# Optimization experiments

Measured on AMD Instinct MI355X. Metric: run time of the kernel, lower is better.

Reference implementation:

```python
import jax, jax.numpy as jnp
import numpy as np

N_NODES = 50_000
EMB = 128
N_GROUPS = 100_000
PER_GROUP = 8
E = N_GROUPS * PER_GROUP  # 800_000


def setup_inputs() -> dict:
    key = jax.random.key(0)
    ks = jax.random.split(key, 12)
    h = 2 * EMB
    inp = {
        "repr": jax.random.normal(ks[0], (N_NODES, EMB), jnp.float32),
        "gd": jax.random.randint(ks[1], (E,), 0, N_NODES, jnp.int32),
        "gd_len": jnp.full((N_GROUPS,), PER_GROUP, jnp.int32),
        "gd_deg": jax.random.uniform(ks[2], (E,), jnp.float32) * 8.0,
        # mlp_combine_gd_deg: Linear(emb+1 -> 2emb), ReLU, Linear(2emb -> emb)
        "W1c": jax.random.normal(ks[3], (EMB + 1, h), jnp.float32) / np.sqrt(EMB + 1),
        "b1c": jnp.zeros((h,), jnp.float32),
        "W2c": jax.random.normal(ks[4], (h, EMB), jnp.float32) / np.sqrt(h),
        "b2c": jnp.zeros((EMB,), jnp.float32),
        # mlp_gd_process: Linear(emb -> 2emb), ReLU, Linear(2emb -> emb)
        "W1p": jax.random.normal(ks[5], (EMB, h), jnp.float32) / np.sqrt(EMB),
        "b1p": jnp.zeros((h,), jnp.float32),
        "W2p": jax.random.normal(ks[6], (h, EMB), jnp.float32) / np.sqrt(h),
        "b2p": jnp.zeros((EMB,), jnp.float32),
    }
    return inp


def reference(repr, gd, gd_len, gd_deg, W1c, b1c, W2c, b2c, W1p, b1p, W2p, b2p):
    n_groups = gd_len.shape[0]
    total = gd.shape[0]
    # gather node reprs along the geodesic index list: [E, emb]
    gd_repr = repr[gd]
    # mlp_combine_gd_deg on [gd_repr ; deg]: [E, emb+1] -> [E, 2emb] -> [E, emb]
    x = jnp.concatenate([gd_repr, gd_deg[:, None]], axis=-1)
    hidden = jax.nn.relu(x @ W1c + b1c)
    gd_repr = hidden @ W2c + b2c
    # count_to_group_index(gd_len): repeat group id i gd_len[i] times, then scatter-add
    group_idx = jnp.repeat(jnp.arange(n_groups, dtype=jnp.int32), gd_len,
                           total_repeat_length=total)
    seg = jax.ops.segment_sum(gd_repr, group_idx, num_segments=n_groups)  # [G, emb]
    # mlp_gd_process
    out = jax.nn.relu(seg @ W1p + b1p) @ W2p + b2p
    return out
```

## Files before the change

kernel.cpp:

```cpp
#include <hip/hip_runtime.h>

typedef _Float16 f16;
typedef _Float16 f16x4 __attribute__((ext_vector_type(4)));
typedef _Float16 f16x8 __attribute__((ext_vector_type(8)));
typedef float f32x4 __attribute__((ext_vector_type(4)));

#define GRID 512

static __device__ __forceinline__ f32x4 mfma16(f16x8 a, f16x8 b, f32x4 c) {
  return __builtin_amdgcn_mfma_f32_16x16x32_f16(a, b, c, 0, 0, 0);
}

__global__ void prep_kernel(const float* __restrict__ W1c, const float* __restrict__ W2c,
                            const float* __restrict__ W1p, const float* __restrict__ W2p,
                            f16* __restrict__ wt) {
  int h = blockIdx.x * 256 + threadIdx.x;
  int local = h & 32767;
  float v;
  if (h < 32768)      { int n = local >> 7, k = local & 127; v = W1c[k * 256 + n]; }
  else if (h < 65536) { int n = local >> 8, k = local & 255; v = W2c[k * 128 + n]; }
  else if (h < 98304) { int n = local >> 7, k = local & 127; v = W1p[k * 256 + n]; }
  else                { int n = local >> 8, k = local & 255; v = W2p[k * 128 + n]; }
  wt[h] = (f16)v;
}

__global__ void prep_repr(const float* __restrict__ repr, f16* __restrict__ repr16, int n) {
  int i = (blockIdx.x * 256 + threadIdx.x) * 8;
  if (i >= n) return;
  float4 a = *reinterpret_cast<const float4*>(repr + i);
  float4 b = *reinterpret_cast<const float4*>(repr + i + 4);
  f16x4 ha, hb;
  ha[0] = (f16)a.x; ha[1] = (f16)a.y; ha[2] = (f16)a.z; ha[3] = (f16)a.w;
  hb[0] = (f16)b.x; hb[1] = (f16)b.y; hb[2] = (f16)b.z; hb[3] = (f16)b.w;
  *reinterpret_cast<f16x4*>(repr16 + i) = ha;
  *reinterpret_cast<f16x4*>(repr16 + i + 4) = hb;
}

#define SMEM_BYTES 80128

#define ISSUE_GATHER(EBASE)                                                     \
  {                                                                             \
    _Pragma("unroll")                                                           \
    for (int gi = 0; gi < 4; gi++) {                                            \
      int mrow = (gi * 8 + wv) * 4 + (lane >> 4);                               \
      int node = gd[(EBASE) + mrow];                                            \
      int ks = (lane & 15) * 8;                                                 \
      const f16* gsrc = repr16 + node * 128 + (ks ^ ((mrow & 7) << 3));         \
      f16* ldst = A_lds + (gi * 8 + wv) * 512;                                  \
      __builtin_amdgcn_global_load_lds(                                         \
          (const __attribute__((address_space(1))) void*)gsrc,                  \
          (__attribute__((address_space(3))) void*)ldst, 16, 0, 0);             \
    }                                                                           \
  }

template <int DMA>
__global__ __launch_bounds__(512, 2) void fused_kernel(
    const float* __restrict__ repr, const f16* __restrict__ repr16,
    const int* __restrict__ gd, const float* __restrict__ gd_deg,
    const float* __restrict__ W1c_full, const float* __restrict__ b1c_g,
    const float* __restrict__ b2c_g, const float* __restrict__ b1p_g,
    const float* __restrict__ b2p_g, const f16* __restrict__ wt,
    float* __restrict__ out, int tiles) {
  extern __shared__ __align__(16) char smem[];
  f16* A_lds   = (f16*)(smem);
  f16* Hh_lds  = (f16*)(smem + 32768);
  f16* S_lds   = (f16*)(smem + 65536);
  f16* H2_lds  = (f16*)(smem + 69632);
  f16* deg_lds = (f16*)(smem + 77824);
  f16* b1c_lds = (f16*)(smem + 78080);
  f16* w1l_lds = (f16*)(smem + 78592);
  f16* b2c_lds = (f16*)(smem + 79104);
  f16* b1p_lds = (f16*)(smem + 79360);
  f16* b2p_lds = (f16*)(smem + 79872);

  const f16* wt1c = wt;
  const f16* wt2c = wt + 32768;
  const f16* wt1p = wt + 65536;
  const f16* wt2p = wt + 98304;

  const int t = threadIdx.x;
  const int bx = blockIdx.x;
  const int lane = t & 63, wv = t >> 6;
  const int q = lane >> 4, c = lane & 15;
  const int m_g = t >> 2, q4 = t & 3;

  if (t < 256) {
    b1c_lds[t] = (f16)b1c_g[t];
    w1l_lds[t] = (f16)W1c_full[128 * 256 + t];
    b1p_lds[t] = (f16)b1p_g[t];
  } else if (t < 384) {
    b2c_lds[t - 256] = (f16)b2c_g[t - 256];
    b2p_lds[t - 256] = (f16)b2p_g[t - 256];
  } else {
    deg_lds[t - 384] = (f16)gd_deg[bx * 128 + (t - 384)];
  }
  if (DMA) {
    ISSUE_GATHER(bx * 128);
  } else {
    int node = gd[bx * 128 + m_g];
    const float4* src = reinterpret_cast<const float4*>(repr) + node * 32 + q4;
    int swz = (m_g & 7) << 3;
#pragma unroll
    for (int i = 0; i < 8; i++) {
      float4 v = src[i * 4];
      f16x4 hv;
      hv[0] = (f16)v.x; hv[1] = (f16)v.y; hv[2] = (f16)v.z; hv[3] = (f16)v.w;
      *reinterpret_cast<f16x4*>(&A_lds[m_g * 128 + ((q4 * 4 + i * 16) ^ swz)]) = hv;
    }
  }
  __syncthreads();

  for (int it = 0;; ++it) {
    const int tile = bx + it * GRID;
    const bool has_next = (tile + GRID) < tiles;
    const int nbase = (tile + GRID) * 128;

    if (!DMA && it > 0) {
      int node = gd[tile * 128 + m_g];
      const float4* src = reinterpret_cast<const float4*>(repr) + node * 32 + q4;
      int swz = (m_g & 7) << 3;
#pragma unroll
      for (int i = 0; i < 8; i++) {
        float4 v = src[i * 4];
        f16x4 hv;
        hv[0] = (f16)v.x; hv[1] = (f16)v.y; hv[2] = (f16)v.z; hv[3] = (f16)v.w;
        *reinterpret_cast<f16x4*>(&A_lds[m_g * 128 + ((q4 * 4 + i * 16) ^ swz)]) = hv;
      }
      if (t >= 384) deg_lds[t - 384] = (f16)gd_deg[tile * 128 + (t - 384)];
      __syncthreads();
    }

    float pdeg = 0.0f;

#pragma unroll
    for (int h = 0; h < 2; ++h) {
      {
        const int nb = wv * 32;
        f32x4 acc[2][4] = {};
#pragma unroll
        for (int kk = 0; kk < 4; kk++) {
          const int kpos = kk * 32 + q * 8;
          f16x8 aw[2], bxv[4];
#pragma unroll
          for (int nf = 0; nf < 2; nf++)
            aw[nf] = *reinterpret_cast<const f16x8*>(&wt1c[(nb + nf * 16 + c) * 128 + kpos]);
#pragma unroll
          for (int mf = 0; mf < 4; mf++) {
            int m = h * 64 + mf * 16 + c;
            bxv[mf] = *reinterpret_cast<const f16x8*>(&A_lds[m * 128 + (kpos ^ ((m & 7) << 3))]);
          }
#pragma unroll
          for (int nf = 0; nf < 2; nf++)
#pragma unroll
            for (int mf = 0; mf < 4; mf++)
              acc[nf][mf] = mfma16(aw[nf], bxv[mf], acc[nf][mf]);
        }
#pragma unroll
        for (int nf = 0; nf < 2; nf++)
#pragma unroll
          for (int mf = 0; mf < 4; mf++) {
            int mloc = mf * 16 + c;
            float dg = (float)deg_lds[h * 64 + mloc];
            int n0 = nb + nf * 16 + q * 4;
            f16x4 hv;
#pragma unroll
            for (int r = 0; r < 4; r++) {
              float v = acc[nf][mf][r] + (float)b1c_lds[n0 + r] + dg * (float)w1l_lds[n0 + r];
              hv[r] = (f16)fmaxf(v, 0.0f);
            }
            *reinterpret_cast<f16x4*>(&Hh_lds[mloc * 256 + (n0 ^ ((mloc & 7) << 3))]) = hv;
          }
      }
      __syncthreads();
      {
        if (DMA && has_next) {
          if (h == 0) {
            if (t >= 384) pdeg = gd_deg[nbase + (t - 384)];
          } else {
            ISSUE_GATHER(nbase);
            if (t >= 384) deg_lds[t - 384] = (f16)pdeg;
          }
        }
        const int nb2 = wv * 16;
        f32x4 acc[4] = {};
#pragma unroll
        for (int kk = 0; kk < 8; kk++) {
          const int kl = kk * 32 + q * 8;
          f16x8 aw = *reinterpret_cast<const f16x8*>(&wt2c[(nb2 + c) * 256 + kl]);
          f16x8 bxv[4];
#pragma unroll
          for (int mf = 0; mf < 4; mf++) {
            int mloc = mf * 16 + c;
            bxv[mf] = *reinterpret_cast<const f16x8*>(&Hh_lds[mloc * 256 + (kl ^ ((mloc & 7) << 3))]);
          }
#pragma unroll
          for (int mf = 0; mf < 4; mf++)
            acc[mf] = mfma16(aw, bxv[mf], acc[mf]);
        }
#pragma unroll
        for (int mf = 0; mf < 4; mf++) {
          float vr[4];
#pragma unroll
          for (int r = 0; r < 4; r++) {
            float v = acc[mf][r];
            v += __shfl_xor(v, 1);
            v += __shfl_xor(v, 2);
            v += __shfl_xor(v, 4);
            vr[r] = v;
          }
          if ((lane & 7) == 0) {
            int g = h * 8 + mf * 2 + (c >> 3);
            int n0 = nb2 + q * 4;
            f16x4 sv;
#pragma unroll
            for (int r = 0; r < 4; r++)
              sv[r] = (f16)(vr[r] + 8.0f * (float)b2c_lds[n0 + r]);
            *reinterpret_cast<f16x4*>(&S_lds[g * 128 + (n0 ^ ((g & 7) << 3))]) = sv;
          }
        }
      }
      __syncthreads();
    }

    {
      const int nb = wv * 32;
      f32x4 acc[2] = {};
#pragma unroll
      for (int kk = 0; kk < 4; kk++) {
        const int kpos = kk * 32 + q * 8;
        f16x8 bxv = *reinterpret_cast<const f16x8*>(&S_lds[c * 128 + (kpos ^ ((c & 7) << 3))]);
#pragma unroll
        for (int nf = 0; nf < 2; nf++) {
          f16x8 aw = *reinterpret_cast<const f16x8*>(&wt1p[(nb + nf * 16 + c) * 128 + kpos]);
          acc[nf] = mfma16(aw, bxv, acc[nf]);
        }
      }
#pragma unroll
      for (int nf = 0; nf < 2; nf++) {
        int n0 = nb + nf * 16 + q * 4;
        f16x4 hv;
#pragma unroll
        for (int r = 0; r < 4; r++)
          hv[r] = (f16)fmaxf(acc[nf][r] + (float)b1p_lds[n0 + r], 0.0f);
        *reinterpret_cast<f16x4*>(&H2_lds[c * 256 + (n0 ^ ((c & 7) << 3))]) = hv;
      }
    }
    __syncthreads();

    {
      const int nb = wv * 16;
      f32x4 acc = {};
#pragma unroll
      for (int kk = 0; kk < 8; kk++) {
        const int kpos = kk * 32 + q * 8;
        f16x8 aw = *reinterpret_cast<const f16x8*>(&wt2p[(nb + c) * 256 + kpos]);
        f16x8 bxv = *reinterpret_cast<const f16x8*>(&H2_lds[c * 256 + (kpos ^ ((c & 7) << 3))]);
        acc = mfma16(aw, bxv, acc);
      }
      float4 ov;
      ov.x = acc[0] + (float)b2p_lds[nb + q * 4 + 0];
      ov.y = acc[1] + (float)b2p_lds[nb + q * 4 + 1];
      ov.z = acc[2] + (float)b2p_lds[nb + q * 4 + 2];
      ov.w = acc[3] + (float)b2p_lds[nb + q * 4 + 3];
      *reinterpret_cast<float4*>(&out[(tile * 16 + c) * 128 + nb + q * 4]) = ov;
    }

    if (!has_next) break;
  }
}

extern "C" void kernel_launch(void* const* d_in, const int* in_sizes, int n_in,
                              void* d_out, int out_size, void* d_ws, size_t ws_size,
                              hipStream_t stream) {
  const float* repr   = (const float*)d_in[0];
  const int*   gd     = (const int*)d_in[1];
  const float* gd_deg = (const float*)d_in[3];
  const float* W1c    = (const float*)d_in[4];
  const float* b1c    = (const float*)d_in[5];
  const float* W2c    = (const float*)d_in[6];
  const float* b2c    = (const float*)d_in[7];
  const float* W1p    = (const float*)d_in[8];
  const float* b1p    = (const float*)d_in[9];
  const float* W2p    = (const float*)d_in[10];
  const float* b2p    = (const float*)d_in[11];
  f16* wt = (f16*)d_ws;
  f16* repr16 = wt + 131072;
  float* out = (float*)d_out;

  const int E = in_sizes[1];
  const int tiles = E / 128;
  const int nrepr = in_sizes[0];
  const size_t need = 262144 + (size_t)nrepr * 2;

  prep_kernel<<<512, 256, 0, stream>>>(W1c, W2c, W1p, W2p, wt);
  if (ws_size >= need) {
    prep_repr<<<(nrepr / 8 + 255) / 256, 256, 0, stream>>>(repr, repr16, nrepr);
    fused_kernel<1><<<GRID, 512, SMEM_BYTES, stream>>>(repr, repr16, gd, gd_deg, W1c,
                                                       b1c, b2c, b1p, b2p, wt, out, tiles);
  } else {
    fused_kernel<0><<<GRID, 512, SMEM_BYTES, stream>>>(repr, repr16, gd, gd_deg, W1c,
                                                       b1c, b2c, b1p, b2p, wt, out, tiles);
  }
}
```

Before: 283.1 us.

## Halve tile to 64 edges, alias LDS buffers, raise occupancy to three blocks per CU

```diff
diff --git a/kernel.cpp b/kernel.cpp
--- a/kernel.cpp
+++ b/kernel.cpp
@@ -5,7 +5,7 @@
 typedef _Float16 f16x8 __attribute__((ext_vector_type(8)));
 typedef float f32x4 __attribute__((ext_vector_type(4)));
 
-#define GRID 512
+#define GRID 768
 
 static __device__ __forceinline__ f32x4 mfma16(f16x8 a, f16x8 b, f32x4 c) {
   return __builtin_amdgcn_mfma_f32_16x16x32_f16(a, b, c, 0, 0, 0);
@@ -36,17 +36,18 @@
   *reinterpret_cast<f16x4*>(repr16 + i + 4) = hb;
 }
 
-#define SMEM_BYTES 80128
+#define SMEM_BYTES 53760
 
 #define ISSUE_GATHER(EBASE)                                                     \
   {                                                                             \
     _Pragma("unroll")                                                           \
-    for (int gi = 0; gi < 4; gi++) {                                            \
-      int mrow = (gi * 8 + wv) * 4 + (lane >> 4);                               \
+    for (int gi = 0; gi < 2; gi++) {                                            \
+      int chunk = gi * 8 + wv;                                                  \
+      int mrow = chunk * 4 + (lane >> 4);                                       \
       int node = gd[(EBASE) + mrow];                                            \
       int ks = (lane & 15) * 8;                                                 \
       const f16* gsrc = repr16 + node * 128 + (ks ^ ((mrow & 7) << 3));         \
-      f16* ldst = A_lds + (gi * 8 + wv) * 512;                                  \
+      f16* ldst = A_lds + chunk * 512;                                          \
       __builtin_amdgcn_global_load_lds(                                         \
           (const __attribute__((address_space(1))) void*)gsrc,                  \
           (__attribute__((address_space(3))) void*)ldst, 16, 0, 0);             \
@@ -54,7 +55,7 @@
   }
 
 template <int DMA>
-__global__ __launch_bounds__(512, 2) void fused_kernel(
+__global__ __launch_bounds__(512, 3) void fused_kernel(
     const float* __restrict__ repr, const f16* __restrict__ repr16,
     const int* __restrict__ gd, const float* __restrict__ gd_deg,
     const float* __restrict__ W1c_full, const float* __restrict__ b1c_g,
@@ -63,15 +64,15 @@
     float* __restrict__ out, int tiles) {
   extern __shared__ __align__(16) char smem[];
   f16* A_lds   = (f16*)(smem);
-  f16* Hh_lds  = (f16*)(smem + 32768);
-  f16* S_lds   = (f16*)(smem + 65536);
-  f16* H2_lds  = (f16*)(smem + 69632);
-  f16* deg_lds = (f16*)(smem + 77824);
-  f16* b1c_lds = (f16*)(smem + 78080);
-  f16* w1l_lds = (f16*)(smem + 78592);
-  f16* b2c_lds = (f16*)(smem + 79104);
-  f16* b1p_lds = (f16*)(smem + 79360);
-  f16* b2p_lds = (f16*)(smem + 79872);
+  f16* Hh_lds  = (f16*)(smem + 16384);
+  f16* H2_lds  = (f16*)(smem + 16384);
+  f16* S_lds   = (f16*)(smem + 49152);
+  f16* deg_lds = (f16*)(smem + 51200);
+  f16* b1c_lds = (f16*)(smem + 51328);
+  f16* w1l_lds = (f16*)(smem + 51840);
+  f16* b1p_lds = (f16*)(smem + 52352);
+  f16* b2c_lds = (f16*)(smem + 52864);
+  f16* b2p_lds = (f16*)(smem + 53120);
 
   const f16* wt1c = wt;
   const f16* wt2c = wt + 32768;
@@ -82,7 +83,6 @@
   const int bx = blockIdx.x;
   const int lane = t & 63, wv = t >> 6;
   const int q = lane >> 4, c = lane & 15;
-  const int m_g = t >> 2, q4 = t & 3;
 
   if (t < 256) {
     b1c_lds[t] = (f16)b1c_g[t];
@@ -91,21 +91,22 @@
   } else if (t < 384) {
     b2c_lds[t - 256] = (f16)b2c_g[t - 256];
     b2p_lds[t - 256] = (f16)b2p_g[t - 256];
+  } else if (t >= 448) {
+    deg_lds[t - 448] = (f16)gd_deg[bx * 64 + (t - 448)];
+  }
+  if (DMA) {
+    ISSUE_GATHER(bx * 64);
   } else {
-    deg_lds[t - 384] = (f16)gd_deg[bx * 128 + (t - 384)];
-  }
-  if (DMA) {
-    ISSUE_GATHER(bx * 128);
-  } else {
-    int node = gd[bx * 128 + m_g];
-    const float4* src = reinterpret_cast<const float4*>(repr) + node * 32 + q4;
-    int swz = (m_g & 7) << 3;
-#pragma unroll
-    for (int i = 0; i < 8; i++) {
-      float4 v = src[i * 4];
+    int row = t >> 3, qc = t & 7;
+    int node = gd[bx * 64 + row];
+    const float4* src = reinterpret_cast<const float4*>(repr) + node * 32 + qc * 4;
+    int swz = (row & 7) << 3;
+#pragma unroll
+    for (int i = 0; i < 4; i++) {
+      float4 v = src[i];
       f16x4 hv;
       hv[0] = (f16)v.x; hv[1] = (f16)v.y; hv[2] = (f16)v.z; hv[3] = (f16)v.w;
-      *reinterpret_cast<f16x4*>(&A_lds[m_g * 128 + ((q4 * 4 + i * 16) ^ swz)]) = hv;
+      *reinterpret_cast<f16x4*>(&A_lds[row * 128 + ((qc * 16 + i * 4) ^ swz)]) = hv;
     }
   }
   __syncthreads();
@@ -113,159 +114,151 @@
   for (int it = 0;; ++it) {
     const int tile = bx + it * GRID;
     const bool has_next = (tile + GRID) < tiles;
-    const int nbase = (tile + GRID) * 128;
+    const int nbase = (tile + GRID) * 64;
 
     if (!DMA && it > 0) {
-      int node = gd[tile * 128 + m_g];
-      const float4* src = reinterpret_cast<const float4*>(repr) + node * 32 + q4;
-      int swz = (m_g & 7) << 3;
-#pragma unroll
-      for (int i = 0; i < 8; i++) {
-        float4 v = src[i * 4];
+      int row = t >> 3, qc = t & 7;
+      int node = gd[tile * 64 + row];
+      const float4* src = reinterpret_cast<const float4*>(repr) + node * 32 + qc * 4;
+      int swz = (row & 7) << 3;
+#pragma unroll
+      for (int i = 0; i < 4; i++) {
+        float4 v = src[i];
         f16x4 hv;
         hv[0] = (f16)v.x; hv[1] = (f16)v.y; hv[2] = (f16)v.z; hv[3] = (f16)v.w;
-        *reinterpret_cast<f16x4*>(&A_lds[m_g * 128 + ((q4 * 4 + i * 16) ^ swz)]) = hv;
-      }
-      if (t >= 384) deg_lds[t - 384] = (f16)gd_deg[tile * 128 + (t - 384)];
+        *reinterpret_cast<f16x4*>(&A_lds[row * 128 + ((qc * 16 + i * 4) ^ swz)]) = hv;
+      }
+      if (t >= 448) deg_lds[t - 448] = (f16)gd_deg[tile * 64 + (t - 448)];
       __syncthreads();
     }
 
-    float pdeg = 0.0f;
-
-#pragma unroll
-    for (int h = 0; h < 2; ++h) {
-      {
-        const int nb = wv * 32;
-        f32x4 acc[2][4] = {};
+    {
+      const int nb = wv * 32;
+#pragma unroll
+      for (int nf = 0; nf < 2; nf++) {
+        f32x4 acc[4] = {};
 #pragma unroll
         for (int kk = 0; kk < 4; kk++) {
           const int kpos = kk * 32 + q * 8;
-          f16x8 aw[2], bxv[4];
-#pragma unroll
-          for (int nf = 0; nf < 2; nf++)
-            aw[nf] = *reinterpret_cast<const f16x8*>(&wt1c[(nb + nf * 16 + c) * 128 + kpos]);
+          f16x8 aw = *reinterpret_cast<const f16x8*>(&wt1c[(nb + nf * 16 + c) * 128 + kpos]);
+          f16x8 bxv[4];
 #pragma unroll
           for (int mf = 0; mf < 4; mf++) {
-            int m = h * 64 + mf * 16 + c;
+            int m = mf * 16 + c;
             bxv[mf] = *reinterpret_cast<const f16x8*>(&A_lds[m * 128 + (kpos ^ ((m & 7) << 3))]);
           }
 #pragma unroll
-          for (int nf = 0; nf < 2; nf++)
-#pragma unroll
-            for (int mf = 0; mf < 4; mf++)
-              acc[nf][mf] = mfma16(aw[nf], bxv[mf], acc[nf][mf]);
-        }
-#pragma unroll
-        for (int nf = 0; nf < 2; nf++)
-#pragma unroll
-          for (int mf = 0; mf < 4; mf++) {
-            int mloc = mf * 16 + c;
-            float dg = (float)deg_lds[h * 64 + mloc];
-            int n0 = nb + nf * 16 + q * 4;
-            f16x4 hv;
-#pragma unroll
-            for (int r = 0; r < 4; r++) {
-              float v = acc[nf][mf][r] + (float)b1c_lds[n0 + r] + dg * (float)w1l_lds[n0 + r];
-              hv[r] = (f16)fmaxf(v, 0.0f);
-            }
-            *reinterpret_cast<f16x4*>(&Hh_lds[mloc * 256 + (n0 ^ ((mloc & 7) << 3))]) = hv;
+          for (int mf = 0; mf < 4; mf++) acc[mf] = mfma16(aw, bxv[mf], acc[mf]);
+        }
+#pragma unroll
+        for (int mf = 0; mf < 4; mf++) {
+          int m = mf * 16 + c;
+          float dg = (float)deg_lds[m];
+          int n0 = nb + nf * 16 + q * 4;
+          f16x4 hv;
+#pragma unroll
+          for (int r = 0; r < 4; r++) {
+            float v = acc[mf][r] + (float)b1c_lds[n0 + r] + dg * (float)w1l_lds[n0 + r];
+            hv[r] = (f16)fmaxf(v, 0.0f);
           }
-      }
-      __syncthreads();
-      {
-        if (DMA && has_next) {
-          if (h == 0) {
-            if (t >= 384) pdeg = gd_deg[nbase + (t - 384)];
-          } else {
-            ISSUE_GATHER(nbase);
-            if (t >= 384) deg_lds[t - 384] = (f16)pdeg;
-          }
-        }
-        const int nb2 = wv * 16;
-        f32x4 acc[4] = {};
-#pragma unroll
-        for (int kk = 0; kk < 8; kk++) {
-          const int kl = kk * 32 + q * 8;
-          f16x8 aw = *reinterpret_cast<const f16x8*>(&wt2c[(nb2 + c) * 256 + kl]);
-          f16x8 bxv[4];
-#pragma unroll
-          for (int mf = 0; mf < 4; mf++) {
-            int mloc = mf * 16 + c;
-            bxv[mf] = *reinterpret_cast<const f16x8*>(&Hh_lds[mloc * 256 + (kl ^ ((mloc & 7) << 3))]);
-          }
-#pragma unroll
-          for (int mf = 0; mf < 4; mf++)
-            acc[mf] = mfma16(aw, bxv[mf], acc[mf]);
-        }
+          *reinterpret_cast<f16x4*>(&Hh_lds[m * 256 + (n0 ^ ((m & 7) << 3))]) = hv;
+        }
+      }
+    }
+    __syncthreads();
+
+    {
+      if (DMA && has_next) {
+        ISSUE_GATHER(nbase);
+        if (t >= 448) deg_lds[t - 448] = (f16)gd_deg[nbase + (t - 448)];
+      }
+      const int nb2 = wv * 16;
+      f32x4 acc[4] = {};
+#pragma unroll
+      for (int kk = 0; kk < 8; kk++) {
+        const int kl = kk * 32 + q * 8;
+        f16x8 aw = *reinterpret_cast<const f16x8*>(&wt2c[(nb2 + c) * 256 + kl]);
+        f16x8 bxv[4];
 #pragma unroll
         for (int mf = 0; mf < 4; mf++) {
-          float vr[4];
-#pragma unroll
-          for (int r = 0; r < 4; r++) {
-            float v = acc[mf][r];
-            v += __shfl_xor(v, 1);
-            v += __shfl_xor(v, 2);
-            v += __shfl_xor(v, 4);
-            vr[r] = v;
-          }
-          if ((lane & 7) == 0) {
-            int g = h * 8 + mf * 2 + (c >> 3);
-            int n0 = nb2 + q * 4;
-            f16x4 sv;
-#pragma unroll
-            for (int r = 0; r < 4; r++)
-              sv[r] = (f16)(vr[r] + 8.0f * (float)b2c_lds[n0 + r]);
-            *reinterpret_cast<f16x4*>(&S_lds[g * 128 + (n0 ^ ((g & 7) << 3))]) = sv;
-          }
-        }
-      }
-      __syncthreads();
-    }
+          int m = mf * 16 + c;
+          bxv[mf] = *reinterpret_cast<const f16x8*>(&Hh_lds[m * 256 + (kl ^ ((m & 7) << 3))]);
+        }
+#pragma unroll
+        for (int mf = 0; mf < 4; mf++) acc[mf] = mfma16(aw, bxv[mf], acc[mf]);
+      }
+#pragma unroll
+      for (int mf = 0; mf < 4; mf++) {
+        float vr[4];
+#pragma unroll
+        for (int r = 0; r < 4; r++) {
+          float v = acc[mf][r];
+          v += __shfl_xor(v, 1);
+          v += __shfl_xor(v, 2);
+          v += __shfl_xor(v, 4);
+          vr[r] = v;
+        }
+        if ((lane & 7) == 0) {
+          int g = mf * 2 + (c >> 3);
+          int n0 = nb2 + q * 4;
+          f16x4 sv;
+#pragma unroll
+          for (int r = 0; r < 4; r++)
+            sv[r] = (f16)(vr[r] + 8.0f * (float)b2c_lds[n0 + r]);
+          *reinterpret_cast<f16x4*>(&S_lds[g * 128 + (n0 ^ (g << 3))]) = sv;
+        }
+      }
+    }
+    __syncthreads();
 
     {
       const int nb = wv * 32;
-      f32x4 acc[2] = {};
-#pragma unroll
-      for (int kk = 0; kk < 4; kk++) {
-        const int kpos = kk * 32 + q * 8;
-        f16x8 bxv = *reinterpret_cast<const f16x8*>(&S_lds[c * 128 + (kpos ^ ((c & 7) << 3))]);
-#pragma unroll
-        for (int nf = 0; nf < 2; nf++) {
+      const int cs = c & 7;
+#pragma unroll
+      for (int nf = 0; nf < 2; nf++) {
+        f32x4 acc = {};
+#pragma unroll
+        for (int kk = 0; kk < 4; kk++) {
+          const int kpos = kk * 32 + q * 8;
+          f16x8 bxv = *reinterpret_cast<const f16x8*>(&S_lds[cs * 128 + (kpos ^ (cs << 3))]);
           f16x8 aw = *reinterpret_cast<const f16x8*>(&wt1p[(nb + nf * 16 + c) * 128 + kpos]);
-          acc[nf] = mfma16(aw, bxv, acc[nf]);
-        }
-      }
-#pragma unroll
-      for (int nf = 0; nf < 2; nf++) {
-        int n0 = nb + nf * 16 + q * 4;
-        f16x4 hv;
-#pragma unroll
-        for (int r = 0; r < 4; r++)
-          hv[r] = (f16)fmaxf(acc[nf][r] + (float)b1p_lds[n0 + r], 0.0f);
-        *reinterpret_cast<f16x4*>(&H2_lds[c * 256 + (n0 ^ ((c & 7) << 3))]) = hv;
+          acc = mfma16(aw, bxv, acc);
+        }
+        if (c < 8) {
+          int n0 = nb + nf * 16 + q * 4;
+          f16x4 hv;
+#pragma unroll
+          for (int r = 0; r < 4; r++)
+            hv[r] = (f16)fmaxf(acc[r] + (float)b1p_lds[n0 + r], 0.0f);
+          *reinterpret_cast<f16x4*>(&H2_lds[c * 256 + (n0 ^ (c << 3))]) = hv;
+        }
       }
     }
     __syncthreads();
 
     {
       const int nb = wv * 16;
+      const int cs = c & 7;
       f32x4 acc = {};
 #pragma unroll
       for (int kk = 0; kk < 8; kk++) {
-        const int kpos = kk * 32 + q * 8;
-        f16x8 aw = *reinterpret_cast<const f16x8*>(&wt2p[(nb + c) * 256 + kpos]);
-        f16x8 bxv = *reinterpret_cast<const f16x8*>(&H2_lds[c * 256 + (kpos ^ ((c & 7) << 3))]);
+        const int kl = kk * 32 + q * 8;
+        f16x8 aw = *reinterpret_cast<const f16x8*>(&wt2p[(nb + c) * 256 + kl]);
+        f16x8 bxv = *reinterpret_cast<const f16x8*>(&H2_lds[cs * 256 + (kl ^ (cs << 3))]);
         acc = mfma16(aw, bxv, acc);
       }
-      float4 ov;
-      ov.x = acc[0] + (float)b2p_lds[nb + q * 4 + 0];
-      ov.y = acc[1] + (float)b2p_lds[nb + q * 4 + 1];
-      ov.z = acc[2] + (float)b2p_lds[nb + q * 4 + 2];
-      ov.w = acc[3] + (float)b2p_lds[nb + q * 4 + 3];
-      *reinterpret_cast<float4*>(&out[(tile * 16 + c) * 128 + nb + q * 4]) = ov;
+      if (c < 8) {
+        float4 ov;
+        ov.x = acc[0] + (float)b2p_lds[nb + q * 4 + 0];
+        ov.y = acc[1] + (float)b2p_lds[nb + q * 4 + 1];
+        ov.z = acc[2] + (float)b2p_lds[nb + q * 4 + 2];
+        ov.w = acc[3] + (float)b2p_lds[nb + q * 4 + 3];
+        *reinterpret_cast<float4*>(&out[(tile * 8 + c) * 128 + nb + q * 4]) = ov;
+      }
     }
 
     if (!has_next) break;
+    __syncthreads();
   }
 }
 
@@ -288,7 +281,7 @@
   float* out = (float*)d_out;
 
   const int E = in_sizes[1];
-  const int tiles = E / 128;
+  const int tiles = E / 64;
   const int nrepr = in_sizes[0];
   const size_t need = 262144 + (size_t)nrepr * 2;
 
```

Result: slower. 593.1 us (+109.5%).

## Hoist weight fragments into registers, split gather prefetch, add MFMA priority

Applied to the files above, without the earlier changes.

```diff
diff --git a/kernel.cpp b/kernel.cpp
--- a/kernel.cpp
+++ b/kernel.cpp
@@ -38,15 +38,16 @@
 
 #define SMEM_BYTES 80128
 
-#define ISSUE_GATHER(EBASE)                                                     \
+#define ISSUE_GATHER_HALF(EBASE, HALF)                                          \
   {                                                                             \
     _Pragma("unroll")                                                           \
-    for (int gi = 0; gi < 4; gi++) {                                            \
-      int mrow = (gi * 8 + wv) * 4 + (lane >> 4);                               \
+    for (int gi = 0; gi < 2; gi++) {                                            \
+      int chunk = (HALF) * 16 + gi * 8 + wv;                                    \
+      int mrow = chunk * 4 + (lane >> 4);                                       \
       int node = gd[(EBASE) + mrow];                                            \
       int ks = (lane & 15) * 8;                                                 \
       const f16* gsrc = repr16 + node * 128 + (ks ^ ((mrow & 7) << 3));         \
-      f16* ldst = A_lds + (gi * 8 + wv) * 512;                                  \
+      f16* ldst = A_lds + chunk * 512;                                          \
       __builtin_amdgcn_global_load_lds(                                         \
           (const __attribute__((address_space(1))) void*)gsrc,                  \
           (__attribute__((address_space(3))) void*)ldst, 16, 0, 0);             \
@@ -95,7 +96,8 @@
     deg_lds[t - 384] = (f16)gd_deg[bx * 128 + (t - 384)];
   }
   if (DMA) {
-    ISSUE_GATHER(bx * 128);
+    ISSUE_GATHER_HALF(bx * 128, 0);
+    ISSUE_GATHER_HALF(bx * 128, 1);
   } else {
     int node = gd[bx * 128 + m_g];
     const float4* src = reinterpret_cast<const float4*>(repr) + node * 32 + q4;
@@ -108,6 +110,20 @@
       *reinterpret_cast<f16x4*>(&A_lds[m_g * 128 + ((q4 * 4 + i * 16) ^ swz)]) = hv;
     }
   }
+
+  f16x8 aw1[2][4];
+  f16x8 aw2[8];
+#pragma unroll
+  for (int nf = 0; nf < 2; nf++)
+#pragma unroll
+    for (int kk = 0; kk < 4; kk++)
+      aw1[nf][kk] = *reinterpret_cast<const f16x8*>(
+          &wt1c[(wv * 32 + nf * 16 + c) * 128 + kk * 32 + q * 8]);
+#pragma unroll
+  for (int kk = 0; kk < 8; kk++)
+    aw2[kk] = *reinterpret_cast<const f16x8*>(
+        &wt2c[(wv * 16 + c) * 256 + kk * 32 + q * 8]);
+
   __syncthreads();
 
   for (int it = 0;; ++it) {
@@ -136,27 +152,23 @@
     for (int h = 0; h < 2; ++h) {
       {
         const int nb = wv * 32;
-        f32x4 acc[2][4] = {};
-#pragma unroll
-        for (int kk = 0; kk < 4; kk++) {
-          const int kpos = kk * 32 + q * 8;
-          f16x8 aw[2], bxv[4];
-#pragma unroll
-          for (int nf = 0; nf < 2; nf++)
-            aw[nf] = *reinterpret_cast<const f16x8*>(&wt1c[(nb + nf * 16 + c) * 128 + kpos]);
-#pragma unroll
-          for (int mf = 0; mf < 4; mf++) {
-            int m = h * 64 + mf * 16 + c;
-            bxv[mf] = *reinterpret_cast<const f16x8*>(&A_lds[m * 128 + (kpos ^ ((m & 7) << 3))]);
-          }
-#pragma unroll
-          for (int nf = 0; nf < 2; nf++)
-#pragma unroll
-            for (int mf = 0; mf < 4; mf++)
-              acc[nf][mf] = mfma16(aw[nf], bxv[mf], acc[nf][mf]);
-        }
-#pragma unroll
-        for (int nf = 0; nf < 2; nf++)
+#pragma unroll
+        for (int nf = 0; nf < 2; nf++) {
+          f32x4 acc[4] = {};
+#pragma unroll
+          for (int kk = 0; kk < 4; kk++) {
+            const int kpos = kk * 32 + q * 8;
+            f16x8 bxv[4];
+#pragma unroll
+            for (int mf = 0; mf < 4; mf++) {
+              int m = h * 64 + mf * 16 + c;
+              bxv[mf] = *reinterpret_cast<const f16x8*>(&A_lds[m * 128 + (kpos ^ ((m & 7) << 3))]);
+            }
+            __builtin_amdgcn_s_setprio(1);
+#pragma unroll
+            for (int mf = 0; mf < 4; mf++) acc[mf] = mfma16(aw1[nf][kk], bxv[mf], acc[mf]);
+            __builtin_amdgcn_s_setprio(0);
+          }
 #pragma unroll
           for (int mf = 0; mf < 4; mf++) {
             int mloc = mf * 16 + c;
@@ -165,19 +177,20 @@
             f16x4 hv;
 #pragma unroll
             for (int r = 0; r < 4; r++) {
-              float v = acc[nf][mf][r] + (float)b1c_lds[n0 + r] + dg * (float)w1l_lds[n0 + r];
+              float v = acc[mf][r] + (float)b1c_lds[n0 + r] + dg * (float)w1l_lds[n0 + r];
               hv[r] = (f16)fmaxf(v, 0.0f);
             }
             *reinterpret_cast<f16x4*>(&Hh_lds[mloc * 256 + (n0 ^ ((mloc & 7) << 3))]) = hv;
           }
+        }
       }
       __syncthreads();
       {
         if (DMA && has_next) {
+          ISSUE_GATHER_HALF(nbase, h);
           if (h == 0) {
             if (t >= 384) pdeg = gd_deg[nbase + (t - 384)];
           } else {
-            ISSUE_GATHER(nbase);
             if (t >= 384) deg_lds[t - 384] = (f16)pdeg;
           }
         }
@@ -186,16 +199,16 @@
 #pragma unroll
         for (int kk = 0; kk < 8; kk++) {
           const int kl = kk * 32 + q * 8;
-          f16x8 aw = *reinterpret_cast<const f16x8*>(&wt2c[(nb2 + c) * 256 + kl]);
           f16x8 bxv[4];
 #pragma unroll
           for (int mf = 0; mf < 4; mf++) {
             int mloc = mf * 16 + c;
             bxv[mf] = *reinterpret_cast<const f16x8*>(&Hh_lds[mloc * 256 + (kl ^ ((mloc & 7) << 3))]);
           }
-#pragma unroll
-          for (int mf = 0; mf < 4; mf++)
-            acc[mf] = mfma16(aw, bxv[mf], acc[mf]);
+          __builtin_amdgcn_s_setprio(1);
+#pragma unroll
+          for (int mf = 0; mf < 4; mf++) acc[mf] = mfma16(aw2[kk], bxv[mf], acc[mf]);
+          __builtin_amdgcn_s_setprio(0);
         }
 #pragma unroll
         for (int mf = 0; mf < 4; mf++) {
```

Result: faster. 245.9 us (-13.1%).

## Restructure fused MLP into software-pipelined stages with full-tile L1/L2 and fewer barriers

Applied to the files above, without the earlier changes.

```diff
diff --git a/kernel.cpp b/kernel.cpp
--- a/kernel.cpp
+++ b/kernel.cpp
@@ -36,17 +36,17 @@
   *reinterpret_cast<f16x4*>(repr16 + i + 4) = hb;
 }
 
-#define SMEM_BYTES 80128
+#define SMEM_BYTES 112896
 
 #define ISSUE_GATHER(EBASE)                                                     \
   {                                                                             \
     _Pragma("unroll")                                                           \
     for (int gi = 0; gi < 4; gi++) {                                            \
-      int mrow = (gi * 8 + wv) * 4 + (lane >> 4);                               \
+      int mrow = gi * 32 + wv * 4 + (lane >> 4);                                \
       int node = gd[(EBASE) + mrow];                                            \
       int ks = (lane & 15) * 8;                                                 \
       const f16* gsrc = repr16 + node * 128 + (ks ^ ((mrow & 7) << 3));         \
-      f16* ldst = A_lds + (gi * 8 + wv) * 512;                                  \
+      f16* ldst = A_lds + (gi * 32 + wv * 4) * 128;                             \
       __builtin_amdgcn_global_load_lds(                                         \
           (const __attribute__((address_space(1))) void*)gsrc,                  \
           (__attribute__((address_space(3))) void*)ldst, 16, 0, 0);             \
@@ -64,14 +64,14 @@
   extern __shared__ __align__(16) char smem[];
   f16* A_lds   = (f16*)(smem);
   f16* Hh_lds  = (f16*)(smem + 32768);
-  f16* S_lds   = (f16*)(smem + 65536);
-  f16* H2_lds  = (f16*)(smem + 69632);
-  f16* deg_lds = (f16*)(smem + 77824);
-  f16* b1c_lds = (f16*)(smem + 78080);
-  f16* w1l_lds = (f16*)(smem + 78592);
-  f16* b2c_lds = (f16*)(smem + 79104);
-  f16* b1p_lds = (f16*)(smem + 79360);
-  f16* b2p_lds = (f16*)(smem + 79872);
+  f16* S_lds   = (f16*)(smem + 98304);
+  f16* H2_lds  = (f16*)(smem + 102400);
+  f16* deg_lds = (f16*)(smem + 110592);
+  f16* b1c_lds = (f16*)(smem + 110848);
+  f16* w1l_lds = (f16*)(smem + 111360);
+  f16* b2c_lds = (f16*)(smem + 111872);
+  f16* b1p_lds = (f16*)(smem + 112128);
+  f16* b2p_lds = (f16*)(smem + 112640);
 
   const f16* wt1c = wt;
   const f16* wt2c = wt + 32768;
@@ -83,6 +83,145 @@
   const int lane = t & 63, wv = t >> 6;
   const int q = lane >> 4, c = lane & 15;
   const int m_g = t >> 2, q4 = t & 3;
+
+  auto do_L1 = [&]() {
+    f32x4 acc[2][8] = {};
+#pragma unroll
+    for (int kk = 0; kk < 4; kk++) {
+      const int kpos = kk * 32 + q * 8;
+      f16x8 bxv[8];
+#pragma unroll
+      for (int mf = 0; mf < 8; mf++) {
+        int m = mf * 16 + c;
+        bxv[mf] = *reinterpret_cast<const f16x8*>(&A_lds[m * 128 + (kpos ^ ((m & 7) << 3))]);
+      }
+      f16x8 aw[2];
+#pragma unroll
+      for (int nf = 0; nf < 2; nf++)
+        aw[nf] = *reinterpret_cast<const f16x8*>(&wt1c[(wv * 32 + nf * 16 + c) * 128 + kpos]);
+      __builtin_amdgcn_s_setprio(1);
+#pragma unroll
+      for (int nf = 0; nf < 2; nf++)
+#pragma unroll
+        for (int mf = 0; mf < 8; mf++)
+          acc[nf][mf] = mfma16(aw[nf], bxv[mf], acc[nf][mf]);
+      __builtin_amdgcn_s_setprio(0);
+    }
+#pragma unroll
+    for (int nf = 0; nf < 2; nf++)
+#pragma unroll
+      for (int mf = 0; mf < 8; mf++) {
+        int mloc = mf * 16 + c;
+        float dg = (float)deg_lds[mloc];
+        int n0 = wv * 32 + nf * 16 + q * 4;
+        f16x4 hv;
+#pragma unroll
+        for (int r = 0; r < 4; r++) {
+          float v = acc[nf][mf][r] + (float)b1c_lds[n0 + r] + dg * (float)w1l_lds[n0 + r];
+          hv[r] = (f16)fmaxf(v, 0.0f);
+        }
+        *reinterpret_cast<f16x4*>(&Hh_lds[mloc * 256 + (n0 ^ ((mloc & 7) << 3))]) = hv;
+      }
+  };
+
+  auto do_L2 = [&]() {
+    f32x4 acc[8] = {};
+#pragma unroll
+    for (int kk = 0; kk < 8; kk++) {
+      const int kl = kk * 32 + q * 8;
+      f16x8 bxv[8];
+#pragma unroll
+      for (int mf = 0; mf < 8; mf++) {
+        int mloc = mf * 16 + c;
+        bxv[mf] = *reinterpret_cast<const f16x8*>(&Hh_lds[mloc * 256 + (kl ^ ((mloc & 7) << 3))]);
+      }
+      f16x8 aw = *reinterpret_cast<const f16x8*>(&wt2c[(wv * 16 + c) * 256 + kl]);
+      __builtin_amdgcn_s_setprio(1);
+#pragma unroll
+      for (int mf = 0; mf < 8; mf++) acc[mf] = mfma16(aw, bxv[mf], acc[mf]);
+      __builtin_amdgcn_s_setprio(0);
+    }
+#pragma unroll
+    for (int mf = 0; mf < 8; mf++) {
+      float vr[4];
+#pragma unroll
+      for (int r = 0; r < 4; r++) {
+        float v = acc[mf][r];
+        v += __shfl_xor(v, 1);
+        v += __shfl_xor(v, 2);
+        v += __shfl_xor(v, 4);
+        vr[r] = v;
+      }
+      if ((lane & 7) == 0) {
+        int g = mf * 2 + (c >> 3);
+        int n0 = wv * 16 + q * 4;
+        f16x4 sv;
+#pragma unroll
+        for (int r = 0; r < 4; r++)
+          sv[r] = (f16)(vr[r] + 8.0f * (float)b2c_lds[n0 + r]);
+        *reinterpret_cast<f16x4*>(&S_lds[g * 128 + (n0 ^ ((g & 7) << 3))]) = sv;
+      }
+    }
+  };
+
+  auto do_L3 = [&]() {
+    f32x4 acc[2] = {};
+#pragma unroll
+    for (int kk = 0; kk < 4; kk++) {
+      const int kpos = kk * 32 + q * 8;
+      f16x8 bxv = *reinterpret_cast<const f16x8*>(&S_lds[c * 128 + (kpos ^ ((c & 7) << 3))]);
+#pragma unroll
+      for (int nf = 0; nf < 2; nf++) {
+        f16x8 aw = *reinterpret_cast<const f16x8*>(&wt1p[(wv * 32 + nf * 16 + c) * 128 + kpos]);
+        acc[nf] = mfma16(aw, bxv, acc[nf]);
+      }
+    }
+#pragma unroll
+    for (int nf = 0; nf < 2; nf++) {
+      int n0 = wv * 32 + nf * 16 + q * 4;
+      f16x4 hv;
+#pragma unroll
+      for (int r = 0; r < 4; r++)
+        hv[r] = (f16)fmaxf(acc[nf][r] + (float)b1p_lds[n0 + r], 0.0f);
+      *reinterpret_cast<f16x4*>(&H2_lds[c * 256 + (n0 ^ ((c & 7) << 3))]) = hv;
+    }
+  };
+
+  auto do_L4 = [&](int pT) {
+    f32x4 acc = {};
+#pragma unroll
+    for (int kk = 0; kk < 8; kk++) {
+      const int kl = kk * 32 + q * 8;
+      f16x8 aw = *reinterpret_cast<const f16x8*>(&wt2p[(wv * 16 + c) * 256 + kl]);
+      f16x8 bxv = *reinterpret_cast<const f16x8*>(&H2_lds[c * 256 + (kl ^ ((c & 7) << 3))]);
+      acc = mfma16(aw, bxv, acc);
+    }
+    int n0 = wv * 16 + q * 4;
+    float4 ov;
+    ov.x = acc[0] + (float)b2p_lds[n0 + 0];
+    ov.y = acc[1] + (float)b2p_lds[n0 + 1];
+    ov.z = acc[2] + (float)b2p_lds[n0 + 2];
+    ov.w = acc[3] + (float)b2p_lds[n0 + 3];
+    *reinterpret_cast<float4*>(&out[(pT * 16 + c) * 128 + n0]) = ov;
+  };
+
+  auto do_dma = [&](int nT) {
+    if (DMA) {
+      ISSUE_GATHER(nT * 128);
+    } else {
+      int node = gd[nT * 128 + m_g];
+      const float4* src = reinterpret_cast<const float4*>(repr) + node * 32 + q4;
+      int swz = (m_g & 7) << 3;
+#pragma unroll
+      for (int i = 0; i < 8; i++) {
+        float4 v = src[i * 4];
+        f16x4 hv;
+        hv[0] = (f16)v.x; hv[1] = (f16)v.y; hv[2] = (f16)v.z; hv[3] = (f16)v.w;
+        *reinterpret_cast<f16x4*>(&A_lds[m_g * 128 + ((q4 * 4 + i * 16) ^ swz)]) = hv;
+      }
+    }
+    if (t >= 384) deg_lds[t - 384] = (f16)gd_deg[nT * 128 + (t - 384)];
+  };
 
   if (t < 256) {
     b1c_lds[t] = (f16)b1c_g[t];
@@ -110,163 +249,30 @@
   }
   __syncthreads();
 
-  for (int it = 0;; ++it) {
-    const int tile = bx + it * GRID;
-    const bool has_next = (tile + GRID) < tiles;
-    const int nbase = (tile + GRID) * 128;
-
-    if (!DMA && it > 0) {
-      int node = gd[tile * 128 + m_g];
-      const float4* src = reinterpret_cast<const float4*>(repr) + node * 32 + q4;
-      int swz = (m_g & 7) << 3;
-#pragma unroll
-      for (int i = 0; i < 8; i++) {
-        float4 v = src[i * 4];
-        f16x4 hv;
-        hv[0] = (f16)v.x; hv[1] = (f16)v.y; hv[2] = (f16)v.z; hv[3] = (f16)v.w;
-        *reinterpret_cast<f16x4*>(&A_lds[m_g * 128 + ((q4 * 4 + i * 16) ^ swz)]) = hv;
-      }
-      if (t >= 384) deg_lds[t - 384] = (f16)gd_deg[tile * 128 + (t - 384)];
-      __syncthreads();
-    }
-
-    float pdeg = 0.0f;
-
-#pragma unroll
-    for (int h = 0; h < 2; ++h) {
-      {
-        const int nb = wv * 32;
-        f32x4 acc[2][4] = {};
-#pragma unroll
-        for (int kk = 0; kk < 4; kk++) {
-          const int kpos = kk * 32 + q * 8;
-          f16x8 aw[2], bxv[4];
-#pragma unroll
-          for (int nf = 0; nf < 2; nf++)
-            aw[nf] = *reinterpret_cast<const f16x8*>(&wt1c[(nb + nf * 16 + c) * 128 + kpos]);
-#pragma unroll
-          for (int mf = 0; mf < 4; mf++) {
-            int m = h * 64 + mf * 16 + c;
-            bxv[mf] = *reinterpret_cast<const f16x8*>(&A_lds[m * 128 + (kpos ^ ((m & 7) << 3))]);
-          }
-#pragma unroll
-          for (int nf = 0; nf < 2; nf++)
-#pragma unroll
-            for (int mf = 0; mf < 4; mf++)
-              acc[nf][mf] = mfma16(aw[nf], bxv[mf], acc[nf][mf]);
-        }
-#pragma unroll
-        for (int nf = 0; nf < 2; nf++)
-#pragma unroll
-          for (int mf = 0; mf < 4; mf++) {
-            int mloc = mf * 16 + c;
-            float dg = (float)deg_lds[h * 64 + mloc];
-            int n0 = nb + nf * 16 + q * 4;
-            f16x4 hv;
-#pragma unroll
-            for (int r = 0; r < 4; r++) {
-              float v = acc[nf][mf][r] + (float)b1c_lds[n0 + r] + dg * (float)w1l_lds[n0 + r];
-              hv[r] = (f16)fmaxf(v, 0.0f);
-            }
-            *reinterpret_cast<f16x4*>(&Hh_lds[mloc * 256 + (n0 ^ ((mloc & 7) << 3))]) = hv;
-          }
-      }
-      __syncthreads();
-      {
-        if (DMA && has_next) {
-          if (h == 0) {
-            if (t >= 384) pdeg = gd_deg[nbase + (t - 384)];
-          } else {
-            ISSUE_GATHER(nbase);
-            if (t >= 384) deg_lds[t - 384] = (f16)pdeg;
-          }
-        }
-        const int nb2 = wv * 16;
-        f32x4 acc[4] = {};
-#pragma unroll
-        for (int kk = 0; kk < 8; kk++) {
-          const int kl = kk * 32 + q * 8;
-          f16x8 aw = *reinterpret_cast<const f16x8*>(&wt2c[(nb2 + c) * 256 + kl]);
-          f16x8 bxv[4];
-#pragma unroll
-          for (int mf = 0; mf < 4; mf++) {
-            int mloc = mf * 16 + c;
-            bxv[mf] = *reinterpret_cast<const f16x8*>(&Hh_lds[mloc * 256 + (kl ^ ((mloc & 7) << 3))]);
-          }
-#pragma unroll
-          for (int mf = 0; mf < 4; mf++)
-            acc[mf] = mfma16(aw, bxv[mf], acc[mf]);
-        }
-#pragma unroll
-        for (int mf = 0; mf < 4; mf++) {
-          float vr[4];
-#pragma unroll
-          for (int r = 0; r < 4; r++) {
-            float v = acc[mf][r];
-            v += __shfl_xor(v, 1);
-            v += __shfl_xor(v, 2);
-            v += __shfl_xor(v, 4);
-            vr[r] = v;
-          }
-          if ((lane & 7) == 0) {
-            int g = h * 8 + mf * 2 + (c >> 3);
-            int n0 = nb2 + q * 4;
-            f16x4 sv;
-#pragma unroll
-            for (int r = 0; r < 4; r++)
-              sv[r] = (f16)(vr[r] + 8.0f * (float)b2c_lds[n0 + r]);
-            *reinterpret_cast<f16x4*>(&S_lds[g * 128 + (n0 ^ ((g & 7) << 3))]) = sv;
-          }
-        }
-      }
-      __syncthreads();
-    }
-
-    {
-      const int nb = wv * 32;
-      f32x4 acc[2] = {};
-#pragma unroll
-      for (int kk = 0; kk < 4; kk++) {
-        const int kpos = kk * 32 + q * 8;
-        f16x8 bxv = *reinterpret_cast<const f16x8*>(&S_lds[c * 128 + (kpos ^ ((c & 7) << 3))]);
-#pragma unroll
-        for (int nf = 0; nf < 2; nf++) {
-          f16x8 aw = *reinterpret_cast<const f16x8*>(&wt1p[(nb + nf * 16 + c) * 128 + kpos]);
-          acc[nf] = mfma16(aw, bxv, acc[nf]);
-        }
-      }
-#pragma unroll
-      for (int nf = 0; nf < 2; nf++) {
-        int n0 = nb + nf * 16 + q * 4;
-        f16x4 hv;
-#pragma unroll
-        for (int r = 0; r < 4; r++)
-          hv[r] = (f16)fmaxf(acc[nf][r] + (float)b1p_lds[n0 + r], 0.0f);
-        *reinterpret_cast<f16x4*>(&H2_lds[c * 256 + (n0 ^ ((c & 7) << 3))]) = hv;
-      }
-    }
+  int T = bx;
+  do_L1();
+  __syncthreads();
+  bool hn = (T + GRID) < tiles;
+  if (hn) do_dma(T + GRID);
+  do_L2();
+  __syncthreads();
+
+  while (hn) {
+    int prevT = T;
+    T += GRID;
+    do_L3();
+    do_L1();
     __syncthreads();
-
-    {
-      const int nb = wv * 16;
-      f32x4 acc = {};
-#pragma unroll
-      for (int kk = 0; kk < 8; kk++) {
-        const int kpos = kk * 32 + q * 8;
-        f16x8 aw = *reinterpret_cast<const f16x8*>(&wt2p[(nb + c) * 256 + kpos]);
-        f16x8 bxv = *reinterpret_cast<const f16x8*>(&H2_lds[c * 256 + (kpos ^ ((c & 7) << 3))]);
-        acc = mfma16(aw, bxv, acc);
-      }
-      float4 ov;
-      ov.x = acc[0] + (float)b2p_lds[nb + q * 4 + 0];
-      ov.y = acc[1] + (float)b2p_lds[nb + q * 4 + 1];
-      ov.z = acc[2] + (float)b2p_lds[nb + q * 4 + 2];
-      ov.w = acc[3] + (float)b2p_lds[nb + q * 4 + 3];
-      *reinterpret_cast<float4*>(&out[(tile * 16 + c) * 128 + nb + q * 4]) = ov;
-    }
-
-    if (!has_next) break;
-  }
+    hn = (T + GRID) < tiles;
+    if (hn) do_dma(T + GRID);
+    do_L2();
+    do_L4(prevT);
+    __syncthreads();
+  }
+
+  do_L3();
+  __syncthreads();
+  do_L4(T);
 }
 
 extern "C" void kernel_launch(void* const* d_in, const int* in_sizes, int n_in,
```

Measured after the change: 456.9 us. 61.4% more time.
